# Optimization experiments

Hardware: AMD Instinct MI355X
Metric: run time of the kernel (lower is better)

The kernel has to match this reference:

```python
import jax, jax.numpy as jnp
import numpy as np

H = 256
V_IN = 32000
V_OUT = 32000
T = 2048


def setup_inputs() -> dict:
    key = jax.random.key(0)
    ks = jax.random.split(key, 16)
    s = 1.0 / np.sqrt(H)
    inp = {
        "src": jax.random.randint(ks[0], (T, 1), 0, V_IN, dtype=jnp.int64 if jax.config.jax_enable_x64 else jnp.int32),
        "trg": jax.random.randint(ks[1], (T, 1), 0, V_OUT, dtype=jnp.int64 if jax.config.jax_enable_x64 else jnp.int32),
        "enc_emb": jax.random.normal(ks[2], (V_IN, H), jnp.float32),
        "enc_W_ih": jax.random.uniform(ks[3], (3 * H, H), jnp.float32, -s, s),
        "enc_W_hh": jax.random.uniform(ks[4], (3 * H, H), jnp.float32, -s, s),
        "enc_b_ih": jax.random.uniform(ks[5], (3 * H,), jnp.float32, -s, s),
        "enc_b_hh": jax.random.uniform(ks[6], (3 * H,), jnp.float32, -s, s),
        "dec_emb": jax.random.normal(ks[7], (V_OUT, H), jnp.float32),
        "dec_W_ih": jax.random.uniform(ks[8], (3 * H, H), jnp.float32, -s, s),
        "dec_W_hh": jax.random.uniform(ks[9], (3 * H, H), jnp.float32, -s, s),
        "dec_b_ih": jax.random.uniform(ks[10], (3 * H,), jnp.float32, -s, s),
        "dec_b_hh": jax.random.uniform(ks[11], (3 * H,), jnp.float32, -s, s),
        "out_W": jax.random.uniform(ks[12], (V_OUT, H), jnp.float32, -s, s),
        "out_b": jax.random.uniform(ks[13], (V_OUT,), jnp.float32, -s, s),
    }
    return inp


def _gru_step(x, h, W_ih, W_hh, b_ih, b_hh):
    # PyTorch GRU cell math. x,h: [H]
    gi = W_ih @ x + b_ih          # [3H]
    gh = W_hh @ h + b_hh          # [3H]
    i_r, i_z, i_n = jnp.split(gi, 3)
    h_r, h_z, h_n = jnp.split(gh, 3)
    r = jax.nn.sigmoid(i_r + h_r)
    z = jax.nn.sigmoid(i_z + h_z)
    n = jnp.tanh(i_n + r * h_n)
    return (1.0 - z) * n + z * h


def reference(src, trg, enc_emb, enc_W_ih, enc_W_hh, enc_b_ih, enc_b_hh,
              dec_emb, dec_W_ih, dec_W_hh, dec_b_ih, dec_b_hh, out_W, out_b):
    src_t = src[:, 0]  # [T], batch forced to 1 by .view(1,1,-1)
    trg_t = trg[:, 0]  # [T]
    h0 = jnp.zeros((H,), enc_emb.dtype)

    def step(h, toks):
        s_tok, t_tok = toks
        # encoder step
        h = _gru_step(enc_emb[s_tok], h, enc_W_ih, enc_W_hh, enc_b_ih, enc_b_hh)
        # decoder step (relu on embedding per source)
        x_d = jax.nn.relu(dec_emb[t_tok])
        h = _gru_step(x_d, h, dec_W_ih, dec_W_hh, dec_b_ih, dec_b_hh)
        logits = out_W @ h + out_b          # [V_OUT]
        return h, jax.nn.log_softmax(logits)

    _, outs = jax.lax.scan(step, h0, (src_t, trg_t))
    return outs[:, None, :]  # [T, 1, V_OUT]
```

## Files before the change

kernel.cpp:

```cpp
#include <hip/hip_runtime.h>
#include <hip/hip_bf16.h>

#define T_STEPS 2048
#define HDIM 256
#define VOUT 32000

typedef short short8 __attribute__((ext_vector_type(8)));
typedef float f32x4 __attribute__((ext_vector_type(4)));

#if defined(__has_builtin)
#if __has_builtin(__builtin_amdgcn_sdot4)
#define HAVE_SDOT4 1
#endif
#endif

__device__ __forceinline__ int dot4i8(int a, int b, int c) {
#ifdef HAVE_SDOT4
    return __builtin_amdgcn_sdot4(a, b, c, false);
#else
#pragma unroll
    for (int k = 0; k < 4; ++k) {
        int av = (a << (24 - 8 * k)) >> 24;
        int bv = (b << (24 - 8 * k)) >> 24;
        c += av * bv;
    }
    return c;
#endif
}

__device__ __forceinline__ float fast_sigmoid(float x) {
    return 1.0f / (1.0f + __expf(-x));
}
__device__ __forceinline__ float fast_tanh(float x) {
    float ax = fabsf(x);
    float e = __expf(-2.0f * ax);
    float t = 1.0f - 2.0f * e / (1.0f + e);
    return copysignf(t, x);
}

__global__ void k_quant(const float* __restrict__ W, int* __restrict__ wq,
                        float* __restrict__ sc) {
    int row = blockIdx.x;
    int t = threadIdx.x;
    float4 w = ((const float4*)(W + (size_t)row * HDIM))[t];
    float m = fmaxf(fmaxf(fabsf(w.x), fabsf(w.y)), fmaxf(fabsf(w.z), fabsf(w.w)));
#pragma unroll
    for (int off = 32; off; off >>= 1) m = fmaxf(m, __shfl_xor(m, off));
    float inv = (m > 0.0f) ? 127.0f / m : 0.0f;
    float scale = (m > 0.0f) ? m * (1.0f / 127.0f) : 0.0f;
    int q0 = __float2int_rn(w.x * inv); q0 = max(-127, min(127, q0));
    int q1 = __float2int_rn(w.y * inv); q1 = max(-127, min(127, q1));
    int q2 = __float2int_rn(w.z * inv); q2 = max(-127, min(127, q2));
    int q3 = __float2int_rn(w.w * inv); q3 = max(-127, min(127, q3));
    int packed = (q0 & 255) | ((q1 & 255) << 8) | ((q2 & 255) << 16) | ((q3 & 255) << 24);
    wq[row * 64 + t] = packed;
    if (t == 0) sc[row] = scale;
}

__global__ __launch_bounds__(256) void k_cvt(const float* __restrict__ in,
                                             unsigned short* __restrict__ out, int n4) {
    int i = blockIdx.x * 256 + threadIdx.x;
    if (i < n4) {
        float4 v = ((const float4*)in)[i];
        unsigned int u[4] = {__float_as_uint(v.x), __float_as_uint(v.y),
                             __float_as_uint(v.z), __float_as_uint(v.w)};
        ushort4 o;
        o.x = (unsigned short)((u[0] + 0x7FFFu + ((u[0] >> 16) & 1)) >> 16);
        o.y = (unsigned short)((u[1] + 0x7FFFu + ((u[1] >> 16) & 1)) >> 16);
        o.z = (unsigned short)((u[2] + 0x7FFFu + ((u[2] >> 16) & 1)) >> 16);
        o.w = (unsigned short)((u[3] + 0x7FFFu + ((u[3] >> 16) & 1)) >> 16);
        ((ushort4*)out)[i] = o;
    }
}

__global__ __launch_bounds__(256) void k_gi(const int* __restrict__ toks,
                                            const float* __restrict__ emb,
                                            const float* __restrict__ W,
                                            const float* __restrict__ b,
                                            float* __restrict__ gi, int do_relu) {
    __shared__ float4 xs[64];
    int t = blockIdx.x;
    int tid = threadIdx.x;
    int tok = toks[t];
    if (tid < 64) {
        float4 x = ((const float4*)(emb + (size_t)tok * HDIM))[tid];
        if (do_relu) {
            x.x = fmaxf(x.x, 0.0f); x.y = fmaxf(x.y, 0.0f);
            x.z = fmaxf(x.z, 0.0f); x.w = fmaxf(x.w, 0.0f);
        }
        xs[tid] = x;
    }
    __syncthreads();
#pragma unroll
    for (int g = 0; g < 3; ++g) {
        int row = tid + g * 256;
        const float4* wr = (const float4*)(W + (size_t)row * HDIM);
        float acc = b[row];
#pragma unroll 16
        for (int k = 0; k < 64; ++k) {
            float4 w = wr[k];
            float4 x = xs[k];
            acc += w.x * x.x + w.y * x.y + w.z * x.z + w.w * x.w;
        }
        gi[(size_t)t * 768 + row] = acc;
    }
}

__global__ __launch_bounds__(768, 3) void k_gru(
    const int* __restrict__ wq_e, const float* __restrict__ sc_e,
    const float* __restrict__ bhh_e, const float* __restrict__ gi_e,
    const int* __restrict__ wq_d, const float* __restrict__ sc_d,
    const float* __restrict__ bhh_d, const float* __restrict__ gi_d,
    float* __restrict__ h_all) {
    __shared__ float Y[768];
    __shared__ float GN[256];
    __shared__ __align__(16) int HQ[64];

    const int tid = threadIdx.x;
    const int w = tid >> 6;
    const int l = tid & 63;
    const int c = l & 3;
    const int g = l >> 2;

    int we[4][16], wd[4][16];
#pragma unroll
    for (int j = 0; j < 4; ++j) {
        const int4* pe = (const int4*)(wq_e + ((w * 64 + g * 4 + j) * 64 + c * 16));
        const int4* pd = (const int4*)(wq_d + ((w * 64 + g * 4 + j) * 64 + c * 16));
#pragma unroll
        for (int i = 0; i < 4; ++i) {
            int4 a = pe[i];
            we[j][4 * i + 0] = a.x; we[j][4 * i + 1] = a.y;
            we[j][4 * i + 2] = a.z; we[j][4 * i + 3] = a.w;
            int4 bq = pd[i];
            wd[j][4 * i + 0] = bq.x; wd[j][4 * i + 1] = bq.y;
            wd[j][4 * i + 2] = bq.z; wd[j][4 * i + 3] = bq.w;
        }
    }
    const float se = sc_e[tid] * (1.0f / 127.0f);
    const float sd = sc_d[tid] * (1.0f / 127.0f);
    const float be = bhh_e[tid];
    const float bd = bhh_d[tid];
    const bool lead = (tid < 256);
    const int c0 = c & 1;
    const int c1 = c & 2;
    float h = 0.0f;
    if (tid < 64) HQ[tid] = 0;
    __syncthreads();

    const float* ge = gi_e + tid;
    const float* gd = gi_d + tid;
    float* hop = h_all + tid;
    const int4* hq4 = (const int4*)HQ;

    for (int t = 0; t < T_STEPS; ++t) {
        float gie = *ge; ge += 768;
        float gid = *gd; gd += 768;

        {
            int4 h0 = hq4[c * 4 + 0];
            int4 h1 = hq4[c * 4 + 1];
            int4 h2 = hq4[c * 4 + 2];
            int4 h3 = hq4[c * 4 + 3];
            int p[4];
#pragma unroll
            for (int j = 0; j < 4; ++j) {
                int a = 0;
                a = dot4i8(we[j][0], h0.x, a);  a = dot4i8(we[j][1], h0.y, a);
                a = dot4i8(we[j][2], h0.z, a);  a = dot4i8(we[j][3], h0.w, a);
                a = dot4i8(we[j][4], h1.x, a);  a = dot4i8(we[j][5], h1.y, a);
                a = dot4i8(we[j][6], h1.z, a);  a = dot4i8(we[j][7], h1.w, a);
                a = dot4i8(we[j][8], h2.x, a);  a = dot4i8(we[j][9], h2.y, a);
                a = dot4i8(we[j][10], h2.z, a); a = dot4i8(we[j][11], h2.w, a);
                a = dot4i8(we[j][12], h3.x, a); a = dot4i8(we[j][13], h3.y, a);
                a = dot4i8(we[j][14], h3.z, a); a = dot4i8(we[j][15], h3.w, a);
                p[j] = a;
            }
            int s0 = c0 ? p[0] : p[1];
            int s1 = c0 ? p[2] : p[3];
            int r0 = (c0 ? p[1] : p[0]) + __shfl_xor(s0, 1);
            int r1 = (c0 ? p[3] : p[2]) + __shfl_xor(s1, 1);
            int s2 = c1 ? r0 : r1;
            int fin = (c1 ? r1 : r0) + __shfl_xor(s2, 2);
            float y = se * (float)fin + be;
            if (tid < 512) Y[tid] = y + gie;
            else { Y[tid] = y; GN[tid - 512] = gie; }
        }
        __syncthreads();
        if (lead) {
            float r = fast_sigmoid(Y[tid]);
            float z = fast_sigmoid(Y[256 + tid]);
            float n = fast_tanh(GN[tid] + r * Y[512 + tid]);
            h = (1.0f - z) * n + z * h;
            ((signed char*)HQ)[tid] = (signed char)__float2int_rn(h * 127.0f);
        }
        __syncthreads();

        {
            int4 h0 = hq4[c * 4 + 0];
            int4 h1 = hq4[c * 4 + 1];
            int4 h2 = hq4[c * 4 + 2];
            int4 h3 = hq4[c * 4 + 3];
            int p[4];
#pragma unroll
            for (int j = 0; j < 4; ++j) {
                int a = 0;
                a = dot4i8(wd[j][0], h0.x, a);  a = dot4i8(wd[j][1], h0.y, a);
                a = dot4i8(wd[j][2], h0.z, a);  a = dot4i8(wd[j][3], h0.w, a);
                a = dot4i8(wd[j][4], h1.x, a);  a = dot4i8(wd[j][5], h1.y, a);
                a = dot4i8(wd[j][6], h1.z, a);  a = dot4i8(wd[j][7], h1.w, a);
                a = dot4i8(wd[j][8], h2.x, a);  a = dot4i8(wd[j][9], h2.y, a);
                a = dot4i8(wd[j][10], h2.z, a); a = dot4i8(wd[j][11], h2.w, a);
                a = dot4i8(wd[j][12], h3.x, a); a = dot4i8(wd[j][13], h3.y, a);
                a = dot4i8(wd[j][14], h3.z, a); a = dot4i8(wd[j][15], h3.w, a);
                p[j] = a;
            }
            int s0 = c0 ? p[0] : p[1];
            int s1 = c0 ? p[2] : p[3];
            int r0 = (c0 ? p[1] : p[0]) + __shfl_xor(s0, 1);
            int r1 = (c0 ? p[3] : p[2]) + __shfl_xor(s1, 1);
            int s2 = c1 ? r0 : r1;
            int fin = (c1 ? r1 : r0) + __shfl_xor(s2, 2);
            float y = sd * (float)fin + bd;
            if (tid < 512) Y[tid] = y + gid;
            else { Y[tid] = y; GN[tid - 512] = gid; }
        }
        __syncthreads();
        if (lead) {
            float r = fast_sigmoid(Y[tid]);
            float z = fast_sigmoid(Y[256 + tid]);
            float n = fast_tanh(GN[tid] + r * Y[512 + tid]);
            h = (1.0f - z) * n + z * h;
            *hop = h; hop += 256;
            ((signed char*)HQ)[tid] = (signed char)__float2int_rn(h * 127.0f);
        }
        __syncthreads();
    }
}

__global__ __launch_bounds__(256) void k_logits(const unsigned short* __restrict__ hb,
                                                const unsigned short* __restrict__ wb,
                                                const float* __restrict__ out_b,
                                                float* __restrict__ out) {
    const int vb = blockIdx.x * 64;
    const int tb = blockIdx.y * 64;
    const int w = threadIdx.x >> 6;
    const int l = threadIdx.x & 63;
    const int m = l & 15;
    const int q = l >> 4;

    const unsigned short* aptr = hb + (size_t)(tb + w * 16 + m) * HDIM + q * 8;
    const unsigned short* bptr = wb + (size_t)(vb + m) * HDIM + q * 8;

    short8 af[8];
#pragma unroll
    for (int kt = 0; kt < 8; ++kt) af[kt] = *(const short8*)(aptr + kt * 32);

    f32x4 acc[4];
#pragma unroll
    for (int nt = 0; nt < 4; ++nt)
#pragma unroll
        for (int r = 0; r < 4; ++r) acc[nt][r] = 0.0f;

#pragma unroll
    for (int nt = 0; nt < 4; ++nt) {
        const unsigned short* bp = bptr + (size_t)nt * 16 * HDIM;
#pragma unroll
        for (int kt = 0; kt < 8; ++kt) {
            short8 bf = *(const short8*)(bp + kt * 32);
            acc[nt] = __builtin_amdgcn_mfma_f32_16x16x32_bf16(af[kt], bf, acc[nt], 0, 0, 0);
        }
    }
#pragma unroll
    for (int nt = 0; nt < 4; ++nt) {
        float bias = out_b[vb + nt * 16 + m];
#pragma unroll
        for (int r = 0; r < 4; ++r) {
            out[(size_t)(tb + w * 16 + q * 4 + r) * VOUT + vb + nt * 16 + m] =
                acc[nt][r] + bias;
        }
    }
}

__global__ __launch_bounds__(256) void k_lse(const float* __restrict__ out,
                                             float* __restrict__ lse) {
    const int t = blockIdx.x;
    const int tid = threadIdx.x;
    const float* rowp = out + (size_t)t * VOUT;
    float m = -3.0e38f, l = 0.0f;
    for (int v = tid; v < VOUT; v += 256) {
        float x = rowp[v];
        float M = fmaxf(m, x);
        l = l * __expf(m - M) + __expf(x - M);
        m = M;
    }
#pragma unroll
    for (int off = 32; off; off >>= 1) {
        float m2 = __shfl_xor(m, off);
        float l2 = __shfl_xor(l, off);
        float M = fmaxf(m, m2);
        l = l * __expf(m - M) + l2 * __expf(m2 - M);
        m = M;
    }
    __shared__ float sm[4], sl[4];
    int lane = tid & 63, wv = tid >> 6;
    if (lane == 0) { sm[wv] = m; sl[wv] = l; }
    __syncthreads();
    if (tid == 0) {
        float M = fmaxf(fmaxf(sm[0], sm[1]), fmaxf(sm[2], sm[3]));
        float L = sl[0] * __expf(sm[0] - M) + sl[1] * __expf(sm[1] - M) +
                  sl[2] * __expf(sm[2] - M) + sl[3] * __expf(sm[3] - M);
        lse[t] = M + __logf(L);
    }
}

__global__ __launch_bounds__(256) void k_sub(float* __restrict__ out,
                                             const float* __restrict__ lse) {
    const int t = blockIdx.y;
    const int v4 = blockIdx.x * 256 + threadIdx.x;
    if (v4 < VOUT / 4) {
        float s = lse[t];
        float4* p = (float4*)(out + (size_t)t * VOUT) + v4;
        float4 o = *p;
        o.x -= s; o.y -= s; o.z -= s; o.w -= s;
        *p = o;
    }
}

extern "C" void kernel_launch(void* const* d_in, const int* in_sizes, int n_in,
                              void* d_out, int out_size, void* d_ws, size_t ws_size,
                              hipStream_t stream) {
    (void)in_sizes; (void)n_in; (void)out_size; (void)ws_size;
    const int*   src      = (const int*)d_in[0];
    const int*   trg      = (const int*)d_in[1];
    const float* enc_emb  = (const float*)d_in[2];
    const float* enc_W_ih = (const float*)d_in[3];
    const float* enc_W_hh = (const float*)d_in[4];
    const float* enc_b_ih = (const float*)d_in[5];
    const float* enc_b_hh = (const float*)d_in[6];
    const float* dec_emb  = (const float*)d_in[7];
    const float* dec_W_ih = (const float*)d_in[8];
    const float* dec_W_hh = (const float*)d_in[9];
    const float* dec_b_ih = (const float*)d_in[10];
    const float* dec_b_hh = (const float*)d_in[11];
    const float* out_W    = (const float*)d_in[12];
    const float* out_b    = (const float*)d_in[13];
    float* out = (float*)d_out;

    char* ws = (char*)d_ws;
    float* gi_e  = (float*)ws; ws += (size_t)T_STEPS * 768 * 4;
    float* gi_d  = (float*)ws; ws += (size_t)T_STEPS * 768 * 4;
    float* h_all = (float*)ws; ws += (size_t)T_STEPS * HDIM * 4;
    float* lse   = (float*)ws; ws += (size_t)T_STEPS * 4;
    float* sc_e  = (float*)ws; ws += 768 * 4;
    float* sc_d  = (float*)ws; ws += 768 * 4;
    int*   wq_e  = (int*)ws;   ws += 768 * 64 * 4;
    int*   wq_d  = (int*)ws;   ws += 768 * 64 * 4;
    unsigned short* h_bf = (unsigned short*)ws; ws += (size_t)T_STEPS * HDIM * 2;
    unsigned short* w_bf = (unsigned short*)ws; ws += (size_t)VOUT * HDIM * 2;

    k_quant<<<768, 64, 0, stream>>>(enc_W_hh, wq_e, sc_e);
    k_quant<<<768, 64, 0, stream>>>(dec_W_hh, wq_d, sc_d);
    k_cvt<<<(VOUT * HDIM / 4 + 255) / 256, 256, 0, stream>>>(out_W, w_bf, VOUT * HDIM / 4);
    k_gi<<<T_STEPS, 256, 0, stream>>>(src, enc_emb, enc_W_ih, enc_b_ih, gi_e, 0);
    k_gi<<<T_STEPS, 256, 0, stream>>>(trg, dec_emb, dec_W_ih, dec_b_ih, gi_d, 1);
    k_gru<<<1, 768, 0, stream>>>(wq_e, sc_e, enc_b_hh, gi_e,
                                 wq_d, sc_d, dec_b_hh, gi_d, h_all);
    k_cvt<<<(T_STEPS * HDIM / 4 + 255) / 256, 256, 0, stream>>>(h_all, h_bf, T_STEPS * HDIM / 4);
    k_logits<<<dim3(VOUT / 64, T_STEPS / 64), 256, 0, stream>>>(h_bf, w_bf, out_b, out);
    k_lse<<<T_STEPS, 256, 0, stream>>>(out, lse);
    k_sub<<<dim3(32, T_STEPS), 256, 0, stream>>>(out, lse);
}
```

Measured before the change: 4.468 ms.

## Restructure GRU recurrence so each thread pair computes all gates, halving barriers

The single-block GRU kernel is reorganised so each pair of threads owns one hidden unit and computes its r, z and n gate rows. The pair reduces its partial sums with a DPP lane swap, and the gate nonlinearities are applied in registers. This removes the shared Y/GN staging and one barrier per half-step, and double-buffers the quantised hidden state. The kernel also writes bf16 h directly, dropping the separate convert kernel. The cost is 192 weight registers per thread in a 512-thread block, which risks spills or low occupancy.

```diff
diff --git a/kernel.cpp b/kernel.cpp
--- a/kernel.cpp
+++ b/kernel.cpp
@@ -11,6 +11,9 @@
 #if defined(__has_builtin)
 #if __has_builtin(__builtin_amdgcn_sdot4)
 #define HAVE_SDOT4 1
+#endif
+#if __has_builtin(__builtin_amdgcn_mov_dpp)
+#define HAVE_DPP 1
 #endif
 #endif
 
@@ -25,6 +28,14 @@
         c += av * bv;
     }
     return c;
+#endif
+}
+
+__device__ __forceinline__ int pairsum(int x) {
+#ifdef HAVE_DPP
+    return x + __builtin_amdgcn_mov_dpp(x, 0xB1, 0xF, 0xF, true);
+#else
+    return x + __shfl_xor(x, 1);
 #endif
 }
 
@@ -106,29 +117,27 @@
     }
 }
 
-__global__ __launch_bounds__(768, 3) void k_gru(
+__global__ __launch_bounds__(512, 2) void k_gru(
     const int* __restrict__ wq_e, const float* __restrict__ sc_e,
     const float* __restrict__ bhh_e, const float* __restrict__ gi_e,
     const int* __restrict__ wq_d, const float* __restrict__ sc_d,
     const float* __restrict__ bhh_d, const float* __restrict__ gi_d,
-    float* __restrict__ h_all) {
-    __shared__ float Y[768];
-    __shared__ float GN[256];
-    __shared__ __align__(16) int HQ[64];
+    unsigned short* __restrict__ h_bf) {
+    __shared__ __align__(16) int HQ[2][64];
 
     const int tid = threadIdx.x;
-    const int w = tid >> 6;
-    const int l = tid & 63;
-    const int c = l & 3;
-    const int g = l >> 2;
-
-    int we[4][16], wd[4][16];
-#pragma unroll
-    for (int j = 0; j < 4; ++j) {
-        const int4* pe = (const int4*)(wq_e + ((w * 64 + g * 4 + j) * 64 + c * 16));
-        const int4* pd = (const int4*)(wq_d + ((w * 64 + g * 4 + j) * 64 + c * 16));
-#pragma unroll
-        for (int i = 0; i < 4; ++i) {
+    const int rg = tid >> 1;
+    const int c  = tid & 1;
+
+    int we[3][32], wd[3][32];
+    float se[3], sd[3], be[3], bd[3];
+#pragma unroll
+    for (int j = 0; j < 3; ++j) {
+        const int row = rg + j * 256;
+        const int4* pe = (const int4*)(wq_e + (row * 64 + c * 32));
+        const int4* pd = (const int4*)(wq_d + (row * 64 + c * 32));
+#pragma unroll
+        for (int i = 0; i < 8; ++i) {
             int4 a = pe[i];
             we[j][4 * i + 0] = a.x; we[j][4 * i + 1] = a.y;
             we[j][4 * i + 2] = a.z; we[j][4 * i + 3] = a.w;
@@ -136,105 +145,87 @@
             wd[j][4 * i + 0] = bq.x; wd[j][4 * i + 1] = bq.y;
             wd[j][4 * i + 2] = bq.z; wd[j][4 * i + 3] = bq.w;
         }
-    }
-    const float se = sc_e[tid] * (1.0f / 127.0f);
-    const float sd = sc_d[tid] * (1.0f / 127.0f);
-    const float be = bhh_e[tid];
-    const float bd = bhh_d[tid];
-    const bool lead = (tid < 256);
-    const int c0 = c & 1;
-    const int c1 = c & 2;
+        se[j] = sc_e[row] * (1.0f / 127.0f);
+        sd[j] = sc_d[row] * (1.0f / 127.0f);
+        be[j] = bhh_e[row];
+        bd[j] = bhh_d[row];
+    }
+
     float h = 0.0f;
-    if (tid < 64) HQ[tid] = 0;
+    if (tid < 64) HQ[0][tid] = 0;
     __syncthreads();
 
-    const float* ge = gi_e + tid;
-    const float* gd = gi_d + tid;
-    float* hop = h_all + tid;
-    const int4* hq4 = (const int4*)HQ;
+    const float* ge = gi_e + rg;
+    const float* gd = gi_d + rg;
+    unsigned short* hop = h_bf + rg;
+    int cur = 0;
 
     for (int t = 0; t < T_STEPS; ++t) {
-        float gie = *ge; ge += 768;
-        float gid = *gd; gd += 768;
-
         {
-            int4 h0 = hq4[c * 4 + 0];
-            int4 h1 = hq4[c * 4 + 1];
-            int4 h2 = hq4[c * 4 + 2];
-            int4 h3 = hq4[c * 4 + 3];
-            int p[4];
-#pragma unroll
-            for (int j = 0; j < 4; ++j) {
-                int a = 0;
-                a = dot4i8(we[j][0], h0.x, a);  a = dot4i8(we[j][1], h0.y, a);
-                a = dot4i8(we[j][2], h0.z, a);  a = dot4i8(we[j][3], h0.w, a);
-                a = dot4i8(we[j][4], h1.x, a);  a = dot4i8(we[j][5], h1.y, a);
-                a = dot4i8(we[j][6], h1.z, a);  a = dot4i8(we[j][7], h1.w, a);
-                a = dot4i8(we[j][8], h2.x, a);  a = dot4i8(we[j][9], h2.y, a);
-                a = dot4i8(we[j][10], h2.z, a); a = dot4i8(we[j][11], h2.w, a);
-                a = dot4i8(we[j][12], h3.x, a); a = dot4i8(we[j][13], h3.y, a);
-                a = dot4i8(we[j][14], h3.z, a); a = dot4i8(we[j][15], h3.w, a);
-                p[j] = a;
+            float g0 = ge[0], g1 = ge[256], g2 = ge[512]; ge += 768;
+            const int4* hq4 = ((const int4*)HQ[cur]) + c * 8;
+            int p0 = 0, p1 = 0, p2 = 0;
+#pragma unroll
+            for (int i = 0; i < 8; ++i) {
+                int4 v = hq4[i];
+                p0 = dot4i8(we[0][4 * i + 0], v.x, p0);
+                p1 = dot4i8(we[1][4 * i + 0], v.x, p1);
+                p2 = dot4i8(we[2][4 * i + 0], v.x, p2);
+                p0 = dot4i8(we[0][4 * i + 1], v.y, p0);
+                p1 = dot4i8(we[1][4 * i + 1], v.y, p1);
+                p2 = dot4i8(we[2][4 * i + 1], v.y, p2);
+                p0 = dot4i8(we[0][4 * i + 2], v.z, p0);
+                p1 = dot4i8(we[1][4 * i + 2], v.z, p1);
+                p2 = dot4i8(we[2][4 * i + 2], v.z, p2);
+                p0 = dot4i8(we[0][4 * i + 3], v.w, p0);
+                p1 = dot4i8(we[1][4 * i + 3], v.w, p1);
+                p2 = dot4i8(we[2][4 * i + 3], v.w, p2);
             }
-            int s0 = c0 ? p[0] : p[1];
-            int s1 = c0 ? p[2] : p[3];
-            int r0 = (c0 ? p[1] : p[0]) + __shfl_xor(s0, 1);
-            int r1 = (c0 ? p[3] : p[2]) + __shfl_xor(s1, 1);
-            int s2 = c1 ? r0 : r1;
-            int fin = (c1 ? r1 : r0) + __shfl_xor(s2, 2);
-            float y = se * (float)fin + be;
-            if (tid < 512) Y[tid] = y + gie;
-            else { Y[tid] = y; GN[tid - 512] = gie; }
+            int f0 = pairsum(p0), f1 = pairsum(p1), f2 = pairsum(p2);
+            float r = fast_sigmoid(g0 + se[0] * (float)f0 + be[0]);
+            float z = fast_sigmoid(g1 + se[1] * (float)f1 + be[1]);
+            float n = fast_tanh(g2 + r * (se[2] * (float)f2 + be[2]));
+            h = (1.0f - z) * n + z * h;
+            if (c == 0)
+                ((signed char*)HQ[cur ^ 1])[rg] = (signed char)__float2int_rn(h * 127.0f);
         }
         __syncthreads();
-        if (lead) {
-            float r = fast_sigmoid(Y[tid]);
-            float z = fast_sigmoid(Y[256 + tid]);
-            float n = fast_tanh(GN[tid] + r * Y[512 + tid]);
+        cur ^= 1;
+
+        {
+            float g0 = gd[0], g1 = gd[256], g2 = gd[512]; gd += 768;
+            const int4* hq4 = ((const int4*)HQ[cur]) + c * 8;
+            int p0 = 0, p1 = 0, p2 = 0;
+#pragma unroll
+            for (int i = 0; i < 8; ++i) {
+                int4 v = hq4[i];
+                p0 = dot4i8(wd[0][4 * i + 0], v.x, p0);
+                p1 = dot4i8(wd[1][4 * i + 0], v.x, p1);
+                p2 = dot4i8(wd[2][4 * i + 0], v.x, p2);
+                p0 = dot4i8(wd[0][4 * i + 1], v.y, p0);
+                p1 = dot4i8(wd[1][4 * i + 1], v.y, p1);
+                p2 = dot4i8(wd[2][4 * i + 1], v.y, p2);
+                p0 = dot4i8(wd[0][4 * i + 2], v.z, p0);
+                p1 = dot4i8(wd[1][4 * i + 2], v.z, p1);
+                p2 = dot4i8(wd[2][4 * i + 2], v.z, p2);
+                p0 = dot4i8(wd[0][4 * i + 3], v.w, p0);
+                p1 = dot4i8(wd[1][4 * i + 3], v.w, p1);
+                p2 = dot4i8(wd[2][4 * i + 3], v.w, p2);
+            }
+            int f0 = pairsum(p0), f1 = pairsum(p1), f2 = pairsum(p2);
+            float r = fast_sigmoid(g0 + sd[0] * (float)f0 + bd[0]);
+            float z = fast_sigmoid(g1 + sd[1] * (float)f1 + bd[1]);
+            float n = fast_tanh(g2 + r * (sd[2] * (float)f2 + bd[2]));
             h = (1.0f - z) * n + z * h;
-            ((signed char*)HQ)[tid] = (signed char)__float2int_rn(h * 127.0f);
+            if (c == 0) {
+                ((signed char*)HQ[cur ^ 1])[rg] = (signed char)__float2int_rn(h * 127.0f);
+                unsigned int u = __float_as_uint(h);
+                *hop = (unsigned short)((u + 0x7FFFu + ((u >> 16) & 1)) >> 16);
+            }
+            hop += 256;
         }
         __syncthreads();
-
-        {
-            int4 h0 = hq4[c * 4 + 0];
-            int4 h1 = hq4[c * 4 + 1];
-            int4 h2 = hq4[c * 4 + 2];
-            int4 h3 = hq4[c * 4 + 3];
-            int p[4];
-#pragma unroll
-            for (int j = 0; j < 4; ++j) {
-                int a = 0;
-                a = dot4i8(wd[j][0], h0.x, a);  a = dot4i8(wd[j][1], h0.y, a);
-                a = dot4i8(wd[j][2], h0.z, a);  a = dot4i8(wd[j][3], h0.w, a);
-                a = dot4i8(wd[j][4], h1.x, a);  a = dot4i8(wd[j][5], h1.y, a);
-                a = dot4i8(wd[j][6], h1.z, a);  a = dot4i8(wd[j][7], h1.w, a);
-                a = dot4i8(wd[j][8], h2.x, a);  a = dot4i8(wd[j][9], h2.y, a);
-                a = dot4i8(wd[j][10], h2.z, a); a = dot4i8(wd[j][11], h2.w, a);
-                a = dot4i8(wd[j][12], h3.x, a); a = dot4i8(wd[j][13], h3.y, a);
-                a = dot4i8(wd[j][14], h3.z, a); a = dot4i8(wd[j][15], h3.w, a);
-                p[j] = a;
-            }
-            int s0 = c0 ? p[0] : p[1];
-            int s1 = c0 ? p[2] : p[3];
-            int r0 = (c0 ? p[1] : p[0]) + __shfl_xor(s0, 1);
-            int r1 = (c0 ? p[3] : p[2]) + __shfl_xor(s1, 1);
-            int s2 = c1 ? r0 : r1;
-            int fin = (c1 ? r1 : r0) + __shfl_xor(s2, 2);
-            float y = sd * (float)fin + bd;
-            if (tid < 512) Y[tid] = y + gid;
-            else { Y[tid] = y; GN[tid - 512] = gid; }
-        }
-        __syncthreads();
-        if (lead) {
-            float r = fast_sigmoid(Y[tid]);
-            float z = fast_sigmoid(Y[256 + tid]);
-            float n = fast_tanh(GN[tid] + r * Y[512 + tid]);
-            h = (1.0f - z) * n + z * h;
-            *hop = h; hop += 256;
-            ((signed char*)HQ)[tid] = (signed char)__float2int_rn(h * 127.0f);
-        }
-        __syncthreads();
+        cur ^= 1;
     }
 }
 
@@ -350,7 +341,6 @@
     char* ws = (char*)d_ws;
     float* gi_e  = (float*)ws; ws += (size_t)T_STEPS * 768 * 4;
     float* gi_d  = (float*)ws; ws += (size_t)T_STEPS * 768 * 4;
-    float* h_all = (float*)ws; ws += (size_t)T_STEPS * HDIM * 4;
     float* lse   = (float*)ws; ws += (size_t)T_STEPS * 4;
     float* sc_e  = (float*)ws; ws += 768 * 4;
     float* sc_d  = (float*)ws; ws += 768 * 4;
@@ -364,9 +354,8 @@
     k_cvt<<<(VOUT * HDIM / 4 + 255) / 256, 256, 0, stream>>>(out_W, w_bf, VOUT * HDIM / 4);
     k_gi<<<T_STEPS, 256, 0, stream>>>(src, enc_emb, enc_W_ih, enc_b_ih, gi_e, 0);
     k_gi<<<T_STEPS, 256, 0, stream>>>(trg, dec_emb, dec_W_ih, dec_b_ih, gi_d, 1);
-    k_gru<<<1, 768, 0, stream>>>(wq_e, sc_e, enc_b_hh, gi_e,
-                                 wq_d, sc_d, dec_b_hh, gi_d, h_all);
-    k_cvt<<<(T_STEPS * HDIM / 4 + 255) / 256, 256, 0, stream>>>(h_all, h_bf, T_STEPS * HDIM / 4);
+    k_gru<<<1, 512, 0, stream>>>(wq_e, sc_e, enc_b_hh, gi_e,
+                                 wq_d, sc_d, dec_b_hh, gi_d, h_bf);
     k_logits<<<dim3(VOUT / 64, T_STEPS / 64), 256, 0, stream>>>(h_bf, w_bf, out_b, out);
     k_lse<<<T_STEPS, 256, 0, stream>>>(out, lse);
     k_sub<<<dim3(32, T_STEPS), 256, 0, stream>>>(out, lse);
```

Result: faster. 4.171 ms (-6.6%).
